# Performance work log

Measured on AMD Instinct MI355X. Metric: run time of the kernel, lower is better.

The kernel has to match this reference:

```python
import jax, jax.numpy as jnp
import numpy as np
from jax import lax

N_IMG = 2
LEVEL_HW = [(200, 200), (100, 100), (50, 50), (25, 25), (13, 13)]
STRIDES = [4, 8, 16, 32, 64]
SIZES = [32.0, 64.0, 128.0, 256.0, 512.0]
A = 3
LEVEL_SIZES = [A * h * w for h, w in LEVEL_HW]
R = sum(LEVEL_SIZES)  # 159882
PRE_NMS = 1000   # pre_nms_top_n['testing']
POST_NMS = 1000  # post_nms_top_n['testing']
NMS_THRESH = 0.7
SCORE_THRESH = 0.0
MIN_SIZE = 1e-3
IMG_H = IMG_W = 800.0
BBOX_XFORM_CLIP = float(np.log(1000.0 / 16.0))


def _make_anchors():
    ratios = np.array([0.5, 1.0, 2.0])
    h_r = np.sqrt(ratios)
    w_r = 1.0 / h_r
    out = []
    for (h, w), stride, size in zip(LEVEL_HW, STRIDES, SIZES):
        ws = size * w_r
        hs = size * h_r
        base = np.stack([-ws / 2, -hs / 2, ws / 2, hs / 2], 1)  # [A,4]
        sx = (np.arange(w) + 0.5) * stride
        sy = (np.arange(h) + 0.5) * stride
        yy, xx = np.meshgrid(sy, sx, indexing='ij')
        shifts = np.stack([xx.ravel(), yy.ravel(), xx.ravel(), yy.ravel()], 1)  # [H*W,4]
        out.append((shifts[:, None, :] + base[None, :, :]).reshape(-1, 4))
    return np.concatenate(out, 0).astype(np.float32)  # [R,4]


def setup_inputs() -> dict:
    key = jax.random.key(0)
    k1, k2 = jax.random.split(key)
    objectness = jax.random.normal(k1, (N_IMG, R), jnp.float32)
    deltas = jax.random.normal(k2, (N_IMG, R, 4), jnp.float32) * 0.2
    anchors = jnp.asarray(_make_anchors())
    return {"objectness": objectness, "deltas": deltas, "anchors": anchors}


def _decode(deltas, anchors):
    # BoxCoder.decode with weights (1,1,1,1)
    wa = anchors[:, 2] - anchors[:, 0]
    ha = anchors[:, 3] - anchors[:, 1]
    cxa = anchors[:, 0] + 0.5 * wa
    cya = anchors[:, 1] + 0.5 * ha
    dx, dy, dw, dh = deltas[..., 0], deltas[..., 1], deltas[..., 2], deltas[..., 3]
    dw = jnp.minimum(dw, BBOX_XFORM_CLIP)
    dh = jnp.minimum(dh, BBOX_XFORM_CLIP)
    cx = dx * wa + cxa
    cy = dy * ha + cya
    w = jnp.exp(dw) * wa
    h = jnp.exp(dh) * ha
    return jnp.stack([cx - 0.5 * w, cy - 0.5 * h, cx + 0.5 * w, cy + 0.5 * h], -1)


def _nms_single(boxes, scores, lvl, valid):
    # batched_nms via per-level coordinate offset trick
    offs = lvl.astype(boxes.dtype) * (max(IMG_H, IMG_W) + 1.0)
    ob = boxes + offs[:, None]
    s = jnp.where(valid, scores, -1.0)
    order = jnp.argsort(-s)
    b = ob[order]          # offset boxes, score-descending
    raw = boxes[order]     # original boxes
    v = valid[order]
    ss = s[order]
    area = (b[:, 2] - b[:, 0]) * (b[:, 3] - b[:, 1])
    lt = jnp.maximum(b[:, None, :2], b[None, :, :2])
    rb = jnp.minimum(b[:, None, 2:], b[None, :, 2:])
    wh = jnp.clip(rb - lt, 0.0)
    inter = wh[..., 0] * wh[..., 1]
    iou = inter / (area[:, None] + area[None, :] - inter + 1e-9)  # [K,K]
    K = b.shape[0]

    def body(keep, i):
        suppressed = jnp.any(keep & (iou[:, i] > NMS_THRESH))
        keep = keep.at[i].set(v[i] & ~suppressed)
        return keep, None

    keep, _ = lax.scan(body, jnp.zeros((K,), bool), jnp.arange(K))
    # compact kept boxes (score order preserved) into fixed POST_NMS slots
    pos = jnp.where(keep, jnp.minimum(jnp.cumsum(keep) - 1, POST_NMS), POST_NMS)
    out_b = jnp.zeros((POST_NMS + 1, 4), boxes.dtype).at[pos].set(raw)[:POST_NMS]
    out_s = jnp.full((POST_NMS + 1,), -1.0, boxes.dtype).at[pos].set(ss)[:POST_NMS]
    return out_b, out_s


def _forward(objectness, deltas, anchors):
    proposals = _decode(deltas, anchors)  # [N,R,4]
    # per-level topk (pre_nms_top_n)
    idxs = []
    off = 0
    for n in LEVEL_SIZES:
        k = min(PRE_NMS, n)
        _, ti = lax.top_k(objectness[:, off:off + n], k)
        idxs.append(ti + off)
        off += n
    top_idx = jnp.concatenate(idxs, 1)  # [N,K]
    obj = jnp.take_along_axis(objectness, top_idx, 1)
    boxes = jnp.take_along_axis(proposals, top_idx[..., None], 1)
    levels = jnp.concatenate([jnp.full((n,), i, jnp.int32) for i, n in enumerate(LEVEL_SIZES)])
    lvl = levels[top_idx]
    scores = jax.nn.sigmoid(obj)
    # clip_boxes_to_image
    x1 = jnp.clip(boxes[..., 0], 0.0, IMG_W)
    y1 = jnp.clip(boxes[..., 1], 0.0, IMG_H)
    x2 = jnp.clip(boxes[..., 2], 0.0, IMG_W)
    y2 = jnp.clip(boxes[..., 3], 0.0, IMG_H)
    boxes = jnp.stack([x1, y1, x2, y2], -1)
    # remove_small_boxes + score_thresh -> validity mask (fixed shapes)
    valid = (x2 - x1 >= MIN_SIZE) & (y2 - y1 >= MIN_SIZE) & (scores >= SCORE_THRESH)
    return jax.vmap(_nms_single)(boxes, scores, lvl, valid)


def reference(objectness, deltas, anchors):
    return _forward(objectness, deltas, anchors)
```

## Files before the change

### kernel.cpp

```cpp
#include <hip/hip_runtime.h>

typedef unsigned long long u64;
typedef unsigned int u32;

#define R_TOT 159882
#define POST 1000
#define IMG_SZ 800.0f
#define NMS_TH 0.7f
#define BBOX_CLIP 4.135166556742356f
#define LCAP 1024
#define MAGIC 0xA5C83D91u

__device__ __forceinline__ float fadd_(float a, float b){ return __fadd_rn(a,b); }
__device__ __forceinline__ float fsub_(float a, float b){ return __fsub_rn(a,b); }
__device__ __forceinline__ float fmul_(float a, float b){ return __fmul_rn(a,b); }

__device__ __forceinline__ int lvl_len(int l){ const int L[5]={120000,30000,7500,1875,507}; return L[l]; }
__device__ __forceinline__ int lvl_off(int l){ const int L[5]={0,120000,150000,157500,159375}; return L[l]; }
__device__ __forceinline__ int lvl_k(int l){ const int L[5]={1000,1000,1000,1000,507}; return L[l]; }

__device__ __forceinline__ u32 mono_(u32 u){ return (u & 0x80000000u) ? ~u : (u | 0x80000000u); }

__device__ __forceinline__ u64 readlane64(u64 v, int i){
  u32 lo = (u32)__builtin_amdgcn_readlane((int)(u32)v, i);
  u32 hi = (u32)__builtin_amdgcn_readlane((int)(u32)(v >> 32), i);
  return ((u64)hi << 32) | (u64)lo;
}

__global__ __launch_bounds__(512) void k_histcollect(const float* __restrict__ obj,
                                                     int* histsum, u32* Zmark, u32* Dmark,
                                                     int* bstarG, int* remG,
                                                     int* cntg, int* cnt2,
                                                     u64* mainG, u64* LbufG){
  int g = blockIdx.x, sl = blockIdx.y;
  int img = g/5, lvl = g%5;
  int n = lvl_len(lvl), s0 = lvl_off(lvl), k = lvl_k(lvl);
  int tid = threadIdx.x, lane = tid & 63, wid = tid >> 6;
  __shared__ __align__(16) char arena[16384];
  __shared__ int wsum[8];
  __shared__ int sh_bs, sh_rem, lc, lc2, gbase, gbase2;
  int* lh = (int*)arena;

  for (int i = tid; i < 4096; i += 512) lh[i] = 0;
  __syncthreads();
  int lo = (int)((long long)n * sl / 16), hiS = (int)((long long)n * (sl+1) / 16);
  const float* p = obj + img*R_TOT + s0;
  #pragma unroll 4
  for (int e = lo + tid; e < hiS; e += 512){
    u32 mu = mono_(__float_as_uint(p[e]));
    atomicAdd(&lh[(~mu) >> 20], 1);
  }
  __syncthreads();

  if (sl == 0){
    for (int i = tid; i < 4096; i += 512) atomicExch((u32*)&histsum[g*4096 + i], 0u);
    if (tid == 0) atomicExch((u32*)&cntg[g], 0u);
    if (tid == 1) atomicExch((u32*)&cnt2[g], 0u);
    __threadfence();
    __syncthreads();
    if (tid == 0) atomicExch(&Zmark[g], MAGIC);
  }
  if (tid == 0){
    while (atomicAdd(&Zmark[g], 0u) != MAGIC) __builtin_amdgcn_s_sleep(16);
  }
  __syncthreads();
  for (int i = tid; i < 4096; i += 512){
    int v = lh[i];
    if (v) atomicAdd(&histsum[g*4096 + i], v);
  }
  __threadfence();
  __syncthreads();
  if (tid == 0) atomicExch(&Dmark[(g << 4) + sl], MAGIC);
  if (tid == 0){
    for (int s = 0; s < 16; s++)
      while (atomicAdd(&Dmark[(g << 4) + s], 0u) != MAGIC) __builtin_amdgcn_s_sleep(16);
  }
  __syncthreads();

  int h[8];
  {
    int* hb = histsum + g*4096 + 8*tid;
    #pragma unroll
    for (int q = 0; q < 8; q++) h[q] = (int)atomicAdd((u32*)&hb[q], 0u);
  }
  int part = 0;
  #pragma unroll
  for (int q = 0; q < 8; q++) part += h[q];
  int x = part;
  for (int d = 1; d < 64; d <<= 1){ int y = __shfl_up(x, d); if (lane >= d) x += y; }
  if (lane == 63) wsum[wid] = x;
  if (tid == 0){ lc = 0; lc2 = 0; }
  __syncthreads();
  int add = 0;
  for (int w = 0; w < wid; w++) add += wsum[w];
  int incl = x + add, excl = incl - part;
  if (excl < k && k <= incl){
    int cum = excl;
    #pragma unroll
    for (int q = 0; q < 8; q++){
      if (cum + h[q] >= k){
        sh_bs = 8*tid + q; sh_rem = k - cum;
        if (sl == 0){ bstarG[g] = 8*tid + q; remG[g] = k - cum; }
        break;
      }
      cum += h[q];
    }
  }
  __syncthreads();
  int bs = sh_bs;

  u64* lmain = (u64*)arena;
  u64* lbuf2 = (u64*)(arena + 8192);
  __syncthreads();
  #pragma unroll 4
  for (int e = lo + tid; e < hiS; e += 512){
    u32 mu = mono_(__float_as_uint(p[e]));
    u64 key56 = (((u64)(~mu)) << 24) | (u32)(s0 + e);
    int bin = (int)(key56 >> 44);
    if (bin < bs){ int pos = atomicAdd(&lc, 1); lmain[pos] = key56; }
    else if (bin == bs){ int pos = atomicAdd(&lc2, 1); if (pos < 1024) lbuf2[pos] = key56; }
  }
  __syncthreads();
  if (tid == 0){ gbase = atomicAdd(&cntg[g], lc); gbase2 = atomicAdd(&cnt2[g], lc2); }
  __syncthreads();
  int b1 = gbase, c1 = lc;
  for (int i = tid; i < c1; i += 512) mainG[g*1024 + b1 + i] = lmain[i];
  int b2 = gbase2, c2l = lc2 < 1024 ? lc2 : 1024;
  for (int i = tid; i < c2l; i += 512){
    int gp = b2 + i;
    if (gp < LCAP) LbufG[g*LCAP + gp] = lbuf2[i];
  }
}

__global__ __launch_bounds__(1024) void k_seldecode(const float* __restrict__ obj,
                                                    const float4* __restrict__ deltas,
                                                    const float4* __restrict__ anchors,
                                                    const u64* __restrict__ mainG,
                                                    const u64* __restrict__ LbufG,
                                                    const int* __restrict__ cntg,
                                                    const int* __restrict__ cnt2,
                                                    const int* __restrict__ remG,
                                                    const int* __restrict__ bstarG,
                                                    float4* boxL, float* scoreL,
                                                    float4* nbox, u64* okeyN, int* ncnt){
  int g = blockIdx.x, img = g/5, lvl = g%5;
  int s0 = lvl_off(lvl), n = lvl_len(lvl), k = lvl_k(lvl);
  const float* p = obj + img*R_TOT + s0;
  __shared__ u64 Lbuf[LCAP];
  __shared__ u64 mainL[1024];
  __shared__ float4 lbox[1024];
  __shared__ u64 lokey[1024];
  __shared__ unsigned char lval[1024];
  __shared__ int h16[16];
  __shared__ int sh_sc, sh_rem;
  __shared__ u64 sh_thr;
  int tid = threadIdx.x, lane = tid & 63;
  int nb = cntg[g];
  int c2 = cnt2[g];
  int rem = remG[g];
  int bs = bstarG[g];
  mainL[tid] = (tid < nb) ? mainG[g*1024 + tid] : ~0ull;
  if (tid == 0){ sh_sc = 0; sh_rem = rem; }
  int c2c = c2 < LCAP ? c2 : LCAP;
  for (int e = tid; e < c2c; e += 1024) Lbuf[e] = LbufG[g*LCAP + e];
  __syncthreads();
  if (c2 <= LCAP){
    for (int e = tid; e < c2; e += 1024){
      u64 kk = Lbuf[e];
      int rk = 0;
      for (int q = 0; q < c2; q++) rk += (Lbuf[q] < kk) ? 1 : 0;
      if (rk < rem){ int p2 = atomicAdd(&sh_sc, 1); mainL[nb + p2] = kk; }
    }
  } else {
    if (tid == 0) sh_thr = ((u64)bs) << 44;
    __syncthreads();
    for (int shift = 40; shift >= 0; shift -= 4){
      if (tid < 16) h16[tid] = 0;
      __syncthreads();
      u64 pref = sh_thr;
      u64 himask = ~((1ull << (shift+4)) - 1ull);
      for (int e = tid; e < n; e += 1024){
        u32 mu = mono_(__float_as_uint(p[e]));
        u64 kk = (((u64)(~mu)) << 24) | (u32)(s0 + e);
        if ((kk & himask) == (pref & himask)) atomicAdd(&h16[(int)((kk >> shift) & 15)], 1);
      }
      __syncthreads();
      if (tid == 0){
        int r2 = sh_rem, cum = 0;
        for (int d = 0; d < 16; d++){
          int hb = h16[d];
          if (cum + hb >= r2){ sh_thr = pref | ((u64)d << shift); sh_rem = r2 - cum; break; }
          cum += hb;
        }
      }
      __syncthreads();
    }
    u64 thr = sh_thr;
    for (int e = tid; e < n; e += 1024){
      u32 mu = mono_(__float_as_uint(p[e]));
      u64 kk = (((u64)(~mu)) << 24) | (u32)(s0 + e);
      if ((int)(kk >> 44) == bs && kk <= thr){ int p2 = atomicAdd(&sh_sc, 1); mainL[nb + p2] = kk; }
    }
  }
  __syncthreads();
  for (int k2 = 2; k2 <= 1024; k2 <<= 1){
    for (int j = k2 >> 1; j > 0; j >>= 1){
      __syncthreads();
      int i = tid, ixj = i ^ j;
      if (ixj > i){
        u64 a = mainL[i], b = mainL[ixj];
        bool up = (i & k2) == 0;
        if ((a > b) == up){ mainL[i] = b; mainL[ixj] = a; }
      }
    }
  }
  __syncthreads();
  int r = tid, t = g*1024 + r;
  if (r < k){
    int idx = (int)(mainL[r] & 0xFFFFFFu);
    float4 a = anchors[idx];
    float4 d = deltas[img*R_TOT + idx];
    float o = obj[img*R_TOT + idx];
    float wa = fsub_(a.z, a.x), ha = fsub_(a.w, a.y);
    float cxa = fadd_(a.x, fmul_(0.5f, wa)), cya = fadd_(a.y, fmul_(0.5f, ha));
    float dw = fminf(d.z, BBOX_CLIP), dh = fminf(d.w, BBOX_CLIP);
    float cx = fadd_(fmul_(d.x, wa), cxa), cy = fadd_(fmul_(d.y, ha), cya);
    float w  = fmul_(expf(dw), wa),        h  = fmul_(expf(dh), ha);
    float x1 = fsub_(cx, fmul_(0.5f, w)), y1 = fsub_(cy, fmul_(0.5f, h));
    float x2 = fadd_(cx, fmul_(0.5f, w)), y2 = fadd_(cy, fmul_(0.5f, h));
    x1 = fminf(fmaxf(x1, 0.0f), IMG_SZ); y1 = fminf(fmaxf(y1, 0.0f), IMG_SZ);
    x2 = fminf(fmaxf(x2, 0.0f), IMG_SZ); y2 = fminf(fmaxf(y2, 0.0f), IMG_SZ);
    bool valid = (fsub_(x2, x1) >= 1e-3f) && (fsub_(y2, y1) >= 1e-3f);
    float e = expf(-o);
    float sig = __fdiv_rn(1.0f, fadd_(1.0f, e));
    float s = valid ? sig : -1.0f;
    u32 sb = __float_as_uint(s);
    u32 ms = (sb & 0x80000000u) ? ~sb : (sb | 0x80000000u);
    float4 b4 = make_float4(x1, y1, x2, y2);
    boxL[t] = b4;
    scoreL[t] = sig;
    lokey[r] = (((u64)(~ms)) << 32) | (u32)(lvl*1000 + r);
    lbox[r] = b4;
    lval[r] = valid ? 1 : 0;
  } else {
    lval[r] = 0;
  }
  __syncthreads();
  if (tid < 64){
    int cnt = 0;
    float off = (float)lvl * 801.0f;
    for (int base = 0; base < k; base += 64){
      int r2 = base + lane;
      bool v = (r2 < k) && lval[r2];
      float4 b = lbox[r2 < k ? r2 : 0];
      u64 mask = __ballot(v);
      int before = __popcll(mask & ((1ull << lane) - 1ull));
      if (v){
        int pos = cnt + before;
        nbox[g*1024 + pos] = make_float4(fadd_(b.x,off), fadd_(b.y,off), fadd_(b.z,off), fadd_(b.w,off));
        okeyN[g*1024 + pos] = lokey[r2];
      }
      cnt += __popcll(mask);
    }
    if (lane == 0) ncnt[g] = cnt;
  }
}

__global__ __launch_bounds__(64) void k_mask(const float4* __restrict__ nbox,
                                             const int* __restrict__ ncnt,
                                             u64* LTG2){
  int g = blockIdx.x, tr = blockIdx.y, tw = blockIdx.z;
  if (tw > tr) return;
  int m = ncnt[g];
  if (tr*64 >= m) return;
  __shared__ float4 shb[64];
  __shared__ float sharea[64];
  int lane = threadIdx.x;
  if (tw*64 + lane < m){
    float4 b = nbox[g*1024 + tw*64 + lane];
    shb[lane] = b;
    sharea[lane] = fmul_(fsub_(b.z,b.x), fsub_(b.w,b.y));
  }
  __syncthreads();
  int j = tr*64 + lane;
  if (j >= m) return;
  float4 a = nbox[g*1024 + j];
  float areaA = fmul_(fsub_(a.z,a.x), fsub_(a.w,a.y));
  int imax = m - tw*64; if (imax > 64) imax = 64;
  if (tw == tr){
    u64 bitsF = 0;
    for (int ii = lane+1; ii < imax; ii++){
      float4 b = shb[ii];
      float ltx = fmaxf(a.x, b.x), lty = fmaxf(a.y, b.y);
      float rbx = fminf(a.z, b.z), rby = fminf(a.w, b.w);
      float wx = fmaxf(fsub_(rbx, ltx), 0.0f), wy = fmaxf(fsub_(rby, lty), 0.0f);
      float inter = fmul_(wx, wy);
      float den = fadd_(fsub_(fadd_(areaA, sharea[ii]), inter), 1e-9f);
      if (__fdiv_rn(inter, den) > NMS_TH) bitsF |= (1ull << ii);
    }
    LTG2[((size_t)(g*1024 + j))*16 + 15] = bitsF;
  } else {
    u64 bits = 0;
    for (int ii = 0; ii < imax; ii++){
      float4 b = shb[ii];
      float ltx = fmaxf(a.x, b.x), lty = fmaxf(a.y, b.y);
      float rbx = fminf(a.z, b.z), rby = fminf(a.w, b.w);
      float wx = fmaxf(fsub_(rbx, ltx), 0.0f), wy = fmaxf(fsub_(rby, lty), 0.0f);
      float inter = fmul_(wx, wy);
      float den = fadd_(fsub_(fadd_(areaA, sharea[ii]), inter), 1e-9f);
      if (__fdiv_rn(inter, den) > NMS_TH) bits |= (1ull << ii);
    }
    LTG2[((size_t)(g*1024 + j))*16 + tw] = bits;
  }
}

struct ChunkBuf {
  ulonglong2 v0, v1, v2, v3, v4, v5, v6, v7;
  u64 ok;
};

__device__ __forceinline__ void issue_chunk(const u64* __restrict__ LT2,
                                            const u64* __restrict__ oK,
                                            int c, int lane, ChunkBuf& b){
  int row = c*64 + lane;
  const ulonglong2* rp = (const ulonglong2*)(LT2 + (size_t)row*16);
  b.v0 = rp[0]; b.v1 = rp[1]; b.v2 = rp[2]; b.v3 = rp[3];
  b.v4 = rp[4]; b.v5 = rp[5]; b.v6 = rp[6]; b.v7 = rp[7];
  b.ok = oK[row];
}

__device__ __forceinline__ void consume_chunk(const ChunkBuf& b, int c, int m, int lane,
                                              u64* KwR, u64* runsL, int& cnt){
  int row = c*64 + lane;
  bool inr = row < m;
  u64 supp = 0;
  #define TERM(q, val) supp |= (((q) < c) ? (val) : 0ull) & KwR[q];
  TERM(0,  b.v0.x) TERM(1,  b.v0.y) TERM(2,  b.v1.x) TERM(3,  b.v1.y)
  TERM(4,  b.v2.x) TERM(5,  b.v2.y) TERM(6,  b.v3.x) TERM(7,  b.v3.y)
  TERM(8,  b.v4.x) TERM(9,  b.v4.y) TERM(10, b.v5.x) TERM(11, b.v5.y)
  TERM(12, b.v6.x) TERM(13, b.v6.y) TERM(14, b.v7.x)
  #undef TERM
  u64 fwd = inr ? b.v7.y : 0;
  u64 live = __ballot(inr && (supp == 0));
  u64 fz = __ballot(fwd != 0);
  u64 kept = 0;
  while (1){
    u64 lf = live & fz;
    if (!lf){ kept |= live; break; }
    int i = __builtin_ctzll(lf);
    u64 bi = 1ull << i;
    u64 below = live & (bi - 1ull);
    kept |= below | bi;
    live &= ~(below | bi);
    live &= ~readlane64(fwd, i);
  }
  KwR[c] = kept;
  bool kp = (kept >> lane) & 1ull;
  int before = __popcll(kept & ((1ull << lane) - 1ull));
  if (kp) runsL[cnt + before] = b.ok;
  cnt += __popcll(kept);
}

__global__ __launch_bounds__(1024) void k_scanmerge(const u64* __restrict__ LTG2,
                                                    const int* __restrict__ ncnt,
                                                    const u64* __restrict__ okeyN,
                                                    const float4* __restrict__ boxL,
                                                    const float* __restrict__ scoreL,
                                                    float* out){
  int img = blockIdx.x, tid = threadIdx.x, lane = tid & 63, wid = tid >> 6;
  __shared__ u64 runs[5*1024];
  __shared__ u64 Kw[5][16];
  __shared__ int cl[5];
  if (wid < 5){
    int l = wid, g = img*5 + l;
    int m = ncnt[g];
    int nch = (m + 63) >> 6;
    const u64* LT2 = LTG2 + ((size_t)g*1024)*16;
    const u64* oK = okeyN + g*1024;
    u64* KwR = &Kw[l][0];
    u64* runsL = &runs[l*1024];
    int cnt = 0;
    ChunkBuf A, B;
    if (nch > 0){
      issue_chunk(LT2, oK, 0, lane, A);
      int c = 0;
      while (c < nch){
        if (c+1 < nch) issue_chunk(LT2, oK, c+1, lane, B);
        consume_chunk(A, c, m, lane, KwR, runsL, cnt);
        c++;
        if (c >= nch) break;
        if (c+1 < nch) issue_chunk(LT2, oK, c+1, lane, A);
        consume_chunk(B, c, m, lane, KwR, runsL, cnt);
        c++;
      }
    }
    if (lane == 0) cl[l] = cnt;
  } else {
    for (int t = tid - 320; t < POST; t += 704){
      out[img*POST*4 + t*4 + 0] = 0.0f;
      out[img*POST*4 + t*4 + 1] = 0.0f;
      out[img*POST*4 + t*4 + 2] = 0.0f;
      out[img*POST*4 + t*4 + 3] = 0.0f;
      out[2*POST*4 + img*POST + t] = -1.0f;
    }
  }
  __syncthreads();
  for (int idx = tid; idx < 5*1024; idx += 1024){
    int l = idx >> 10, i = idx & 1023;
    if (i < cl[l]){
      u64 key = runs[l*1024 + i];
      int o0 = l+1; if (o0 >= 5) o0 -= 5;
      int o1 = l+2; if (o1 >= 5) o1 -= 5;
      int o2 = l+3; if (o2 >= 5) o2 -= 5;
      int o3 = l+4; if (o3 >= 5) o3 -= 5;
      const u64* r0 = runs + (o0 << 10);
      const u64* r1 = runs + (o1 << 10);
      const u64* r2 = runs + (o2 << 10);
      const u64* r3 = runs + (o3 << 10);
      int lo0 = 0, hi0 = cl[o0];
      int lo1 = 0, hi1 = cl[o1];
      int lo2 = 0, hi2 = cl[o2];
      int lo3 = 0, hi3 = cl[o3];
      #pragma unroll 1
      for (int st = 0; st < 11; st++){
        int m0 = (lo0+hi0)>>1, m1 = (lo1+hi1)>>1, m2 = (lo2+hi2)>>1, m3 = (lo3+hi3)>>1;
        u64 a0 = r0[m0], a1 = r1[m1], a2 = r2[m2], a3 = r3[m3];
        if (lo0 < hi0){ if (a0 < key) lo0 = m0+1; else hi0 = m0; }
        if (lo1 < hi1){ if (a1 < key) lo1 = m1+1; else hi1 = m1; }
        if (lo2 < hi2){ if (a2 < key) lo2 = m2+1; else hi2 = m2; }
        if (lo3 < hi3){ if (a3 < key) lo3 = m3+1; else hi3 = m3; }
      }
      int rank = i + lo0 + lo1 + lo2 + lo3;
      if (rank < POST){
        int pos = (int)(key & 0xFFFFFFFFull);
        int lvl = pos / 1000, r = pos - lvl*1000;
        int gg = img*5 + lvl;
        float4 bo = boxL[gg*1024 + r];
        float sc = scoreL[gg*1024 + r];
        out[img*POST*4 + rank*4 + 0] = bo.x;
        out[img*POST*4 + rank*4 + 1] = bo.y;
        out[img*POST*4 + rank*4 + 2] = bo.z;
        out[img*POST*4 + rank*4 + 3] = bo.w;
        out[2*POST*4 + img*POST + rank] = sc;
      }
    }
  }
}

extern "C" void kernel_launch(void* const* d_in, const int* in_sizes, int n_in,
                              void* d_out, int out_size, void* d_ws, size_t ws_size,
                              hipStream_t stream){
  (void)in_sizes; (void)n_in; (void)out_size; (void)ws_size;
  const float*  obj     = (const float*)d_in[0];
  const float4* deltas  = (const float4*)d_in[1];
  const float4* anchors = (const float4*)d_in[2];
  float* out = (float*)d_out;
  char* ws = (char*)d_ws;
  int* histsum = (int*)(ws + 0);
  u32* Zmark   = (u32*)(ws + 163840);
  u32* Dmark   = (u32*)(ws + 163904);
  int* bstarG  = (int*)(ws + 164544);
  int* remG    = (int*)(ws + 164608);
  int* cntg    = (int*)(ws + 164672);
  int* cnt2    = (int*)(ws + 164736);
  u64* mainG   = (u64*)(ws + 164800);
  u64* LbufG   = (u64*)(ws + 246720);
  float4* boxL = (float4*)(ws + 328640);
  float* scoreL= (float*)(ws + 492480);
  u64* okeyN   = (u64*)(ws + 533440);
  float4* nbox = (float4*)(ws + 615360);
  u64* LTG2    = (u64*)(ws + 779200);
  int* ncnt    = (int*)(ws + 2089920);

  {
    dim3 gh(10, 16);
    k_histcollect<<<gh, 512, 0, stream>>>(obj, histsum, Zmark, Dmark,
                                          bstarG, remG, cntg, cnt2, mainG, LbufG);
  }
  k_seldecode<<<10, 1024, 0, stream>>>(obj, deltas, anchors, mainG, LbufG, cntg, cnt2,
                                       remG, bstarG, boxL, scoreL, nbox, okeyN, ncnt);
  {
    dim3 gm(10, 16, 16);
    k_mask<<<gm, 64, 0, stream>>>(nbox, ncnt, LTG2);
  }
  k_scanmerge<<<2, 1024, 0, stream>>>(LTG2, ncnt, okeyN, boxL, scoreL, out);
}
```

Measured before the change: 169.8 us.

## Replace cross-block histogram sync with redundant per-block full histograms

Each of the 16 slice blocks per (image, level) group now builds the full-level histogram in shared memory itself. Before, the blocks merged partial histograms through global atomics guarded by spin-wait flags. Each slice then writes its candidates and ties to private per-slice buffers, and the select kernel concatenates them using prefix offsets. This removes the global atomics, the inter-block spin barriers and the zeroing pass, at the cost of each block reading the whole level (16x redundant reads of objectness) with 8-wide batched loads. It also drops the reliance on co-resident blocks for the spin barrier.

```diff
diff --git a/kernel.cpp b/kernel.cpp
--- a/kernel.cpp
+++ b/kernel.cpp
@@ -9,7 +9,6 @@
 #define NMS_TH 0.7f
 #define BBOX_CLIP 4.135166556742356f
 #define LCAP 1024
-#define MAGIC 0xA5C83D91u
 
 __device__ __forceinline__ float fadd_(float a, float b){ return __fadd_rn(a,b); }
 __device__ __forceinline__ float fsub_(float a, float b){ return __fsub_rn(a,b); }
@@ -28,68 +27,58 @@
 }
 
 __global__ __launch_bounds__(512) void k_histcollect(const float* __restrict__ obj,
-                                                     int* histsum, u32* Zmark, u32* Dmark,
-                                                     int* bstarG, int* remG,
-                                                     int* cntg, int* cnt2,
-                                                     u64* mainG, u64* LbufG){
+                                                     u64* mainS, u64* tieS,
+                                                     int* cntS, int* cnt2S,
+                                                     int* bstarG, int* remG){
   int g = blockIdx.x, sl = blockIdx.y;
   int img = g/5, lvl = g%5;
   int n = lvl_len(lvl), s0 = lvl_off(lvl), k = lvl_k(lvl);
   int tid = threadIdx.x, lane = tid & 63, wid = tid >> 6;
   __shared__ __align__(16) char arena[16384];
   __shared__ int wsum[8];
-  __shared__ int sh_bs, sh_rem, lc, lc2, gbase, gbase2;
+  __shared__ int sh_bs, sh_rem, lc, lc2;
   int* lh = (int*)arena;
-
   for (int i = tid; i < 4096; i += 512) lh[i] = 0;
   __syncthreads();
-  int lo = (int)((long long)n * sl / 16), hiS = (int)((long long)n * (sl+1) / 16);
   const float* p = obj + img*R_TOT + s0;
-  #pragma unroll 4
-  for (int e = lo + tid; e < hiS; e += 512){
-    u32 mu = mono_(__float_as_uint(p[e]));
-    atomicAdd(&lh[(~mu) >> 20], 1);
-  }
-  __syncthreads();
-
-  if (sl == 0){
-    for (int i = tid; i < 4096; i += 512) atomicExch((u32*)&histsum[g*4096 + i], 0u);
-    if (tid == 0) atomicExch((u32*)&cntg[g], 0u);
-    if (tid == 1) atomicExch((u32*)&cnt2[g], 0u);
-    __threadfence();
-    __syncthreads();
-    if (tid == 0) atomicExch(&Zmark[g], MAGIC);
-  }
-  if (tid == 0){
-    while (atomicAdd(&Zmark[g], 0u) != MAGIC) __builtin_amdgcn_s_sleep(16);
-  }
-  __syncthreads();
-  for (int i = tid; i < 4096; i += 512){
-    int v = lh[i];
-    if (v) atomicAdd(&histsum[g*4096 + i], v);
-  }
-  __threadfence();
-  __syncthreads();
-  if (tid == 0) atomicExch(&Dmark[(g << 4) + sl], MAGIC);
-  if (tid == 0){
-    for (int s = 0; s < 16; s++)
-      while (atomicAdd(&Dmark[(g << 4) + s], 0u) != MAGIC) __builtin_amdgcn_s_sleep(16);
+
+  {
+    int full = n >> 12;
+    for (int it = 0; it < full; it++){
+      int e0 = (it << 12) + tid;
+      float v[8];
+      #pragma unroll
+      for (int q = 0; q < 8; q++) v[q] = p[e0 + (q << 9)];
+      #pragma unroll
+      for (int q = 0; q < 8; q++){
+        u32 mu = mono_(__float_as_uint(v[q]));
+        atomicAdd(&lh[(~mu) >> 20], 1);
+      }
+    }
+    int e0 = (full << 12) + tid;
+    float v[8];
+    #pragma unroll
+    for (int q = 0; q < 8; q++){ int e = e0 + (q << 9); v[q] = (e < n) ? p[e] : 0.0f; }
+    #pragma unroll
+    for (int q = 0; q < 8; q++){
+      int e = e0 + (q << 9);
+      if (e < n){
+        u32 mu = mono_(__float_as_uint(v[q]));
+        atomicAdd(&lh[(~mu) >> 20], 1);
+      }
+    }
   }
   __syncthreads();
 
   int h[8];
-  {
-    int* hb = histsum + g*4096 + 8*tid;
-    #pragma unroll
-    for (int q = 0; q < 8; q++) h[q] = (int)atomicAdd((u32*)&hb[q], 0u);
-  }
+  #pragma unroll
+  for (int q = 0; q < 8; q++) h[q] = lh[8*tid + q];
   int part = 0;
   #pragma unroll
   for (int q = 0; q < 8; q++) part += h[q];
   int x = part;
   for (int d = 1; d < 64; d <<= 1){ int y = __shfl_up(x, d); if (lane >= d) x += y; }
   if (lane == 63) wsum[wid] = x;
-  if (tid == 0){ lc = 0; lc2 = 0; }
   __syncthreads();
   int add = 0;
   for (int w = 0; w < wid; w++) add += wsum[w];
@@ -111,34 +100,58 @@
 
   u64* lmain = (u64*)arena;
   u64* lbuf2 = (u64*)(arena + 8192);
-  __syncthreads();
-  #pragma unroll 4
-  for (int e = lo + tid; e < hiS; e += 512){
-    u32 mu = mono_(__float_as_uint(p[e]));
-    u64 key56 = (((u64)(~mu)) << 24) | (u32)(s0 + e);
-    int bin = (int)(key56 >> 44);
-    if (bin < bs){ int pos = atomicAdd(&lc, 1); lmain[pos] = key56; }
-    else if (bin == bs){ int pos = atomicAdd(&lc2, 1); if (pos < 1024) lbuf2[pos] = key56; }
-  }
-  __syncthreads();
-  if (tid == 0){ gbase = atomicAdd(&cntg[g], lc); gbase2 = atomicAdd(&cnt2[g], lc2); }
-  __syncthreads();
-  int b1 = gbase, c1 = lc;
-  for (int i = tid; i < c1; i += 512) mainG[g*1024 + b1 + i] = lmain[i];
-  int b2 = gbase2, c2l = lc2 < 1024 ? lc2 : 1024;
-  for (int i = tid; i < c2l; i += 512){
-    int gp = b2 + i;
-    if (gp < LCAP) LbufG[g*LCAP + gp] = lbuf2[i];
-  }
+  if (tid == 0){ lc = 0; lc2 = 0; }
+  __syncthreads();
+  int lo = (int)((long long)n * sl / 16), hiS = (int)((long long)n * (sl+1) / 16);
+  int len = hiS - lo;
+  {
+    int full = len >> 12;
+    for (int it = 0; it < full; it++){
+      int e0 = lo + (it << 12) + tid;
+      float v[8];
+      #pragma unroll
+      for (int q = 0; q < 8; q++) v[q] = p[e0 + (q << 9)];
+      #pragma unroll
+      for (int q = 0; q < 8; q++){
+        int e = e0 + (q << 9);
+        u32 mu = mono_(__float_as_uint(v[q]));
+        u64 key56 = (((u64)(~mu)) << 24) | (u32)(s0 + e);
+        int bin = (int)(key56 >> 44);
+        if (bin < bs){ int pos = atomicAdd(&lc, 1); lmain[pos] = key56; }
+        else if (bin == bs){ int pos = atomicAdd(&lc2, 1); if (pos < 1024) lbuf2[pos] = key56; }
+      }
+    }
+    int e0 = lo + (full << 12) + tid;
+    float v[8];
+    #pragma unroll
+    for (int q = 0; q < 8; q++){ int e = e0 + (q << 9); v[q] = (e < hiS) ? p[e] : 0.0f; }
+    #pragma unroll
+    for (int q = 0; q < 8; q++){
+      int e = e0 + (q << 9);
+      if (e < hiS){
+        u32 mu = mono_(__float_as_uint(v[q]));
+        u64 key56 = (((u64)(~mu)) << 24) | (u32)(s0 + e);
+        int bin = (int)(key56 >> 44);
+        if (bin < bs){ int pos = atomicAdd(&lc, 1); lmain[pos] = key56; }
+        else if (bin == bs){ int pos = atomicAdd(&lc2, 1); if (pos < 1024) lbuf2[pos] = key56; }
+      }
+    }
+  }
+  __syncthreads();
+  int idx16 = g*16 + sl;
+  if (tid == 0){ cntS[idx16] = lc; cnt2S[idx16] = lc2; }
+  for (int i = tid; i < lc; i += 512) mainS[idx16*1024 + i] = lmain[i];
+  int c2l = lc2 < 1024 ? lc2 : 1024;
+  for (int i = tid; i < c2l; i += 512) tieS[idx16*1024 + i] = lbuf2[i];
 }
 
 __global__ __launch_bounds__(1024) void k_seldecode(const float* __restrict__ obj,
                                                     const float4* __restrict__ deltas,
                                                     const float4* __restrict__ anchors,
-                                                    const u64* __restrict__ mainG,
-                                                    const u64* __restrict__ LbufG,
-                                                    const int* __restrict__ cntg,
-                                                    const int* __restrict__ cnt2,
+                                                    const u64* __restrict__ mainS,
+                                                    const u64* __restrict__ tieS,
+                                                    const int* __restrict__ cntS,
+                                                    const int* __restrict__ cnt2S,
                                                     const int* __restrict__ remG,
                                                     const int* __restrict__ bstarG,
                                                     float4* boxL, float* scoreL,
@@ -152,17 +165,42 @@
   __shared__ u64 lokey[1024];
   __shared__ unsigned char lval[1024];
   __shared__ int h16[16];
+  __shared__ int scnt[16], tcnt[16];
+  __shared__ int sbase[17], tbase[17];
   __shared__ int sh_sc, sh_rem;
   __shared__ u64 sh_thr;
   int tid = threadIdx.x, lane = tid & 63;
-  int nb = cntg[g];
-  int c2 = cnt2[g];
+  if (tid < 16){ scnt[tid] = cntS[g*16 + tid]; tcnt[tid] = cnt2S[g*16 + tid]; }
+  __syncthreads();
+  if (tid == 0){
+    int s = 0, t2 = 0;
+    #pragma unroll
+    for (int q = 0; q < 16; q++){ sbase[q] = s; s += scnt[q]; tbase[q] = t2; t2 += tcnt[q]; }
+    sbase[16] = s; tbase[16] = t2;
+  }
+  __syncthreads();
+  int nb = sbase[16];
+  int c2 = tbase[16];
   int rem = remG[g];
   int bs = bstarG[g];
-  mainL[tid] = (tid < nb) ? mainG[g*1024 + tid] : ~0ull;
+  {
+    u64 vmain = ~0ull;
+    if (tid < nb){
+      int sl = 0;
+      #pragma unroll
+      for (int q = 1; q < 16; q++) sl += (tid >= sbase[q]) ? 1 : 0;
+      vmain = mainS[(g*16 + sl)*1024 + (tid - sbase[sl])];
+    }
+    mainL[tid] = vmain;
+  }
   if (tid == 0){ sh_sc = 0; sh_rem = rem; }
   int c2c = c2 < LCAP ? c2 : LCAP;
-  for (int e = tid; e < c2c; e += 1024) Lbuf[e] = LbufG[g*LCAP + e];
+  for (int e = tid; e < c2c; e += 1024){
+    int sl = 0;
+    #pragma unroll
+    for (int q = 1; q < 16; q++) sl += (e >= tbase[q]) ? 1 : 0;
+    Lbuf[e] = tieS[(g*16 + sl)*1024 + (e - tbase[sl])];
+  }
   __syncthreads();
   if (c2 <= LCAP){
     for (int e = tid; e < c2; e += 1024){
@@ -456,28 +494,24 @@
   const float4* anchors = (const float4*)d_in[2];
   float* out = (float*)d_out;
   char* ws = (char*)d_ws;
-  int* histsum = (int*)(ws + 0);
-  u32* Zmark   = (u32*)(ws + 163840);
-  u32* Dmark   = (u32*)(ws + 163904);
-  int* bstarG  = (int*)(ws + 164544);
-  int* remG    = (int*)(ws + 164608);
-  int* cntg    = (int*)(ws + 164672);
-  int* cnt2    = (int*)(ws + 164736);
-  u64* mainG   = (u64*)(ws + 164800);
-  u64* LbufG   = (u64*)(ws + 246720);
-  float4* boxL = (float4*)(ws + 328640);
-  float* scoreL= (float*)(ws + 492480);
-  u64* okeyN   = (u64*)(ws + 533440);
-  float4* nbox = (float4*)(ws + 615360);
-  u64* LTG2    = (u64*)(ws + 779200);
-  int* ncnt    = (int*)(ws + 2089920);
+  u64* mainS   = (u64*)(ws + 0);
+  u64* tieS    = (u64*)(ws + 1310720);
+  int* cntS    = (int*)(ws + 2621440);
+  int* cnt2S   = (int*)(ws + 2622080);
+  int* bstarG  = (int*)(ws + 2622720);
+  int* remG    = (int*)(ws + 2622784);
+  float4* boxL = (float4*)(ws + 2622848);
+  float* scoreL= (float*)(ws + 2786688);
+  u64* okeyN   = (u64*)(ws + 2827648);
+  float4* nbox = (float4*)(ws + 2909568);
+  u64* LTG2    = (u64*)(ws + 3073408);
+  int* ncnt    = (int*)(ws + 4384128);
 
   {
     dim3 gh(10, 16);
-    k_histcollect<<<gh, 512, 0, stream>>>(obj, histsum, Zmark, Dmark,
-                                          bstarG, remG, cntg, cnt2, mainG, LbufG);
-  }
-  k_seldecode<<<10, 1024, 0, stream>>>(obj, deltas, anchors, mainG, LbufG, cntg, cnt2,
+    k_histcollect<<<gh, 512, 0, stream>>>(obj, mainS, tieS, cntS, cnt2S, bstarG, remG);
+  }
+  k_seldecode<<<10, 1024, 0, stream>>>(obj, deltas, anchors, mainS, tieS, cntS, cnt2S,
                                        remG, bstarG, boxL, scoreL, nbox, okeyN, ncnt);
   {
     dim3 gm(10, 16, 16);
```

Measured after the change: 150.8 us. 11.2% less time.
